# Kernel tuning notes

Measured on AMD Instinct MI355X. Metric: run time of the kernel, lower is better.

The kernel has to match this reference:

```python
import jax, jax.numpy as jnp
import numpy as np

HIDDEN = 20


def setup_inputs() -> dict:
    key = jax.random.key(0)
    ks = jax.random.split(key, 8)
    B, T = 8192, 2048
    x = jax.random.normal(ks[0], (B, T), dtype=jnp.float32)
    # linear1: 1 -> HIDDEN
    W1 = jax.random.normal(ks[1], (HIDDEN, 1), dtype=jnp.float32) * 0.5
    b1 = jax.random.normal(ks[2], (HIDDEN,), dtype=jnp.float32) * 0.1
    # LSTMCell(HIDDEN, HIDDEN): torch layout [4*H, H], gate order i,f,g,o
    W_ih = jax.random.normal(ks[3], (4 * HIDDEN, HIDDEN), dtype=jnp.float32) * 0.2
    W_hh = jax.random.normal(ks[4], (4 * HIDDEN, HIDDEN), dtype=jnp.float32) * 0.2
    b_ih = jax.random.normal(ks[5], (4 * HIDDEN,), dtype=jnp.float32) * 0.1
    b_hh = jax.random.normal(ks[6], (4 * HIDDEN,), dtype=jnp.float32) * 0.1
    # linear2: HIDDEN -> 1
    W2 = jax.random.normal(ks[7], (1, HIDDEN), dtype=jnp.float32) * 0.2
    b2 = jnp.zeros((1,), dtype=jnp.float32)
    return {"input": x, "W1": W1, "b1": b1, "W_ih": W_ih, "W_hh": W_hh,
            "b_ih": b_ih, "b_hh": b_hh, "W2": W2, "b2": b2}


def reference(input, W1, b1, W_ih, W_hh, b_ih, b_hh, W2, b2):
    B, T = input.shape
    h0 = jnp.zeros((B, HIDDEN), dtype=input.dtype)
    c0 = jnp.zeros((B, HIDDEN), dtype=input.dtype)

    def step(carry, x_t):
        h, c = carry
        # linear1 on scalar input: [B] -> [B, HIDDEN]
        hid = x_t[:, None] * W1[:, 0][None, :] + b1
        # LSTMCell gates, torch order: i, f, g, o
        gates = hid @ W_ih.T + b_ih + h @ W_hh.T + b_hh  # [B, 4H]
        i_g, f_g, g_g, o_g = jnp.split(gates, 4, axis=-1)
        c_new = jax.nn.sigmoid(f_g) * c + jax.nn.sigmoid(i_g) * jnp.tanh(g_g)
        h_new = jax.nn.sigmoid(o_g) * jnp.tanh(c_new)
        out = h_new @ W2.T + b2  # [B, 1]
        return (h_new, c_new), out[:, 0]

    xs = input.T  # [T, B]
    _, outs = jax.lax.scan(step, (h0, c0), xs)  # outs: [T, B]
    return outs.T  # [B, T]
```

## Files before the change

kernel.cpp:

```cpp
#include <hip/hip_runtime.h>


#define HID 20
#define ROWS_PER_WAVE 3
#define NTHREADS 64
#define L2E 1.4426950408889634f

typedef _Float16 v2h __attribute__((ext_vector_type(2)));

__device__ __forceinline__ float exp2_hw(float v) { return __builtin_amdgcn_exp2f(v); }
__device__ __forceinline__ float rcp_hw(float v)  { return __builtin_amdgcn_rcpf(v); }

__device__ __forceinline__ float sig_s(float gs) {
    return rcp_hw(1.0f + exp2_hw(-gs));
}

__device__ __forceinline__ float dot2(v2h w, v2h h, float acc) {
#if __has_builtin(__builtin_amdgcn_fdot2)
    return __builtin_amdgcn_fdot2(w, h, acc, false);
#else
    asm("v_dot2_f32_f16 %0, %1, %2, %0" : "+v"(acc) : "v"(w), "v"(h));
    return acc;
#endif
}

__device__ __forceinline__ v2h u2h(unsigned u) {
    v2h r; __builtin_memcpy(&r, &u, 4); return r;
}

__global__ __attribute__((amdgpu_flat_work_group_size(NTHREADS, NTHREADS),
                          amdgpu_waves_per_eu(3, 3)))
void lstm_wave(
        const float* __restrict__ x,
        const float* __restrict__ W1,
        const float* __restrict__ b1,
        const float* __restrict__ W_ih,
        const float* __restrict__ W_hh,
        const float* __restrict__ b_ih,
        const float* __restrict__ b_hh,
        const float* __restrict__ W2,
        const float* __restrict__ b2,
        float* __restrict__ out,
        const int B, const int T)
{
    const int lane = threadIdx.x;
    const int lrow = lane / HID;
    const int m    = lane % HID;
    const bool outlane = (lrow == 3) && (m < ROWS_PER_WAVE);
    const int rslot = (lrow == 3) ? m : lrow;
    const long rowbase = (long)blockIdx.x * ROWS_PER_WAVE;
    const long row = rowbase + ((lrow == 3) ? (long)((m < 3) ? m : 0) : (long)lrow);
    const long arow = (row < B) ? row : (B - 1);
    const bool ovalid = outlane && (row < B);

    __shared__ __align__(16) _Float16 hbuf[ROWS_PER_WAVE + 1][32];

    float u[4], v[4];
    if (lrow < 3) {
#pragma unroll
        for (int g = 0; g < 4; ++g) {
            const int j = g * HID + m;
            const float s = (g == 2) ? (2.0f * L2E) : L2E;
            float uu = 0.f, vv = 0.f;
#pragma unroll
            for (int k = 0; k < HID; ++k) {
                const float wi = W_ih[j * HID + k];
                uu += wi * W1[k];
                vv += wi * b1[k];
            }
            u[g] = s * uu;
            v[g] = s * (vv + b_ih[j] + b_hh[j]);
        }
    } else {
#pragma unroll
        for (int g = 0; g < 4; ++g) { u[g] = 0.f; v[g] = 0.f; }
        v[0] = b2[0];
    }

    v2h whh[4][HID / 2];
    if (lrow < 3) {
#pragma unroll
        for (int g = 0; g < 4; ++g) {
            const int j = g * HID + m;
            const float s = (g == 2) ? (2.0f * L2E) : L2E;
#pragma unroll
            for (int kk = 0; kk < HID / 2; ++kk) {
                v2h w;
                w.x = (_Float16)(s * W_hh[j * HID + 2 * kk]);
                w.y = (_Float16)(s * W_hh[j * HID + 2 * kk + 1]);
                whh[g][kk] = w;
            }
        }
    } else {
#pragma unroll
        for (int kk = 0; kk < HID / 2; ++kk) {
            v2h w;
            w.x = (_Float16)W2[2 * kk];
            w.y = (_Float16)W2[2 * kk + 1];
            whh[0][kk] = w;
            whh[1][kk] = (v2h)(_Float16)0;
            whh[2][kk] = (v2h)(_Float16)0;
            whh[3][kk] = (v2h)(_Float16)0;
        }
    }

#pragma unroll
    for (int g = 0; g < 4; ++g)
#pragma unroll
        for (int kk = 0; kk < HID / 2; ++kk)
            asm volatile("" : "+v"(whh[g][kk]));

    float cs = 0.f;

    ((_Float16*)hbuf)[lane]      = (_Float16)0;
    ((_Float16*)hbuf)[lane + 64] = (_Float16)0;

    const float* __restrict__ xrow = x   + arow * T;
    float* __restrict__       orow = out + arow * T;

    const uint4* __restrict__ rdp4 = (const uint4*)&hbuf[rslot][0];
    const uint2* __restrict__ rdp2 = (const uint2*)&hbuf[rslot][16];
    _Float16* __restrict__    wrp  = &hbuf[lrow][m];

    v2h hp[HID / 2];
#pragma unroll
    for (int q = 0; q < HID / 2; ++q) hp[q] = (v2h)(_Float16)0;

    float4 xq = *(const float4*)&xrow[0];
    float4 xq_next;
    float4 obuf = make_float4(0.f, 0.f, 0.f, 0.f);

#define BODY(XV, OSLOT)                                                         \
    {                                                                           \
        const float xv = (XV);                                                  \
        float a0 = fmaf(xv, u[0], v[0]);                                        \
        float a1 = fmaf(xv, u[1], v[1]);                                        \
        float a2 = fmaf(xv, u[2], v[2]);                                        \
        float a3 = fmaf(xv, u[3], v[3]);                                        \
        _Pragma("unroll")                                                       \
        for (int q = 0; q < HID / 2; ++q) {                                     \
            a0 = dot2(whh[0][q], hp[q], a0);                                    \
            a1 = dot2(whh[1][q], hp[q], a1);                                    \
            a2 = dot2(whh[2][q], hp[q], a2);                                    \
            a3 = dot2(whh[3][q], hp[q], a3);                                    \
        }                                                                       \
        __builtin_amdgcn_s_setprio(1);                                          \
        OSLOT = a0;                                                             \
        const float fg  = sig_s(a1);                                            \
        const float e0i = exp2_hw(-a0);                                         \
        const float e2  = exp2_hw(a2);                                          \
        const float P1  = (1.0f + e0i) * (1.0f + e2);                           \
        const float igg = (2.0f * L2E) * (e2 - 1.0f) * rcp_hw(P1);              \
        cs = fg * cs + igg;                                                     \
        const float e3i = exp2_hw(-a3);                                         \
        const float ec  = exp2_hw(cs);                                          \
        const float P2  = (1.0f + e3i) * (1.0f + ec);                           \
        *wrp = (_Float16)((ec - 1.0f) * rcp_hw(P2));                            \
        const uint4 Ra = rdp4[0];                                               \
        const uint4 Rb = rdp4[1];                                               \
        const uint2 Rc = *rdp2;                                                 \
        __builtin_amdgcn_s_setprio(0);                                          \
        hp[0] = u2h(Ra.x); hp[1] = u2h(Ra.y); hp[2] = u2h(Ra.z);                \
        hp[3] = u2h(Ra.w); hp[4] = u2h(Rb.x); hp[5] = u2h(Rb.y);                \
        hp[6] = u2h(Rb.z); hp[7] = u2h(Rb.w); hp[8] = u2h(Rc.x);                \
        hp[9] = u2h(Rc.y);                                                      \
    }

    for (int t = 0; t < T; t += 4) {
        const int tp = (t + 4 < T) ? (t + 4) : t;
        xq_next = *(const float4*)&xrow[tp];

        BODY(xq.x, obuf.w)
        if (t >= 4 && ovalid) *(float4*)&orow[t - 4] = obuf;
        BODY(xq.y, obuf.x)
        BODY(xq.z, obuf.y)
        BODY(xq.w, obuf.z)

        xq = xq_next;
    }

    {
        float o = v[0];
#pragma unroll
        for (int q = 0; q < HID / 2; ++q)
            o = dot2(whh[0][q], hp[q], o);
        obuf.w = o;
        if (ovalid) *(float4*)&orow[T - 4] = obuf;
    }
#undef BODY
}

extern "C" void kernel_launch(void* const* d_in, const int* in_sizes, int n_in,
                              void* d_out, int out_size, void* d_ws, size_t ws_size,
                              hipStream_t stream) {
    (void)n_in; (void)d_ws; (void)ws_size; (void)out_size;
    const float* x    = (const float*)d_in[0];
    const float* W1   = (const float*)d_in[1];
    const float* b1   = (const float*)d_in[2];
    const float* W_ih = (const float*)d_in[3];
    const float* W_hh = (const float*)d_in[4];
    const float* b_ih = (const float*)d_in[5];
    const float* b_hh = (const float*)d_in[6];
    const float* W2   = (const float*)d_in[7];
    const float* b2   = (const float*)d_in[8];
    float* out        = (float*)d_out;

    const int B = 8192;
    const int T = in_sizes[0] / B;
    const int grid = (B + ROWS_PER_WAVE - 1) / ROWS_PER_WAVE;

    lstm_wave<<<grid, NTHREADS, 0, stream>>>(x, W1, b1, W_ih, W_hh, b_ih, b_hh, W2, b2, out, B, T);
}
```

Measured before the change: 957.6 us.

## Pack six batch rows per wave with two hidden units per lane

Remaps lanes so each lane owns two hidden units (10 lanes per row), fitting six batch rows per 64-lane wave instead of three. The output projection is folded into every lane's dot loop, and hidden states are exchanged as packed half2 words in LDS. This halves the number of waves and the serial per-step overhead per row, but doubles per-lane register weights and dependent work. Occupancy is lowered to 2 waves per EU to make room for the larger register footprint.

Measured after the change: 1.251 ms. 30.6% more time.

```diff
diff --git a/kernel.cpp b/kernel.cpp
--- a/kernel.cpp
+++ b/kernel.cpp
@@ -2,7 +2,8 @@
 
 
 #define HID 20
-#define ROWS_PER_WAVE 3
+#define LPR 10
+#define RPW 6
 #define NTHREADS 64
 #define L2E 1.4426950408889634f
 
@@ -27,9 +28,12 @@
 __device__ __forceinline__ v2h u2h(unsigned u) {
     v2h r; __builtin_memcpy(&r, &u, 4); return r;
 }
+__device__ __forceinline__ unsigned h2u(v2h h) {
+    unsigned r; __builtin_memcpy(&r, &h, 4); return r;
+}
 
 __global__ __attribute__((amdgpu_flat_work_group_size(NTHREADS, NTHREADS),
-                          amdgpu_waves_per_eu(3, 3)))
+                          amdgpu_waves_per_eu(2, 2)))
 void lstm_wave(
         const float* __restrict__ x,
         const float* __restrict__ W1,
@@ -44,118 +48,156 @@
         const int B, const int T)
 {
     const int lane = threadIdx.x;
-    const int lrow = lane / HID;
-    const int m    = lane % HID;
-    const bool outlane = (lrow == 3) && (m < ROWS_PER_WAVE);
-    const int rslot = (lrow == 3) ? m : lrow;
-    const long rowbase = (long)blockIdx.x * ROWS_PER_WAVE;
-    const long row = rowbase + ((lrow == 3) ? (long)((m < 3) ? m : 0) : (long)lrow);
-    const long arow = (row < B) ? row : (B - 1);
-    const bool ovalid = outlane && (row < B);
-
-    __shared__ __align__(16) _Float16 hbuf[ROWS_PER_WAVE + 1][32];
-
-    float u[4], v[4];
-    if (lrow < 3) {
+    const int r    = lane / LPR;
+    const int mlo  = lane % LPR;
+    const bool gatelane = (r < RPW);
+    const int rslot = gatelane ? r : (lane - 60);
+
+    int outr = -1;
+    if (lane >= 60)      outr = lane - 60;
+    else if (lane == 40) outr = 4;
+    else if (lane == 50) outr = 5;
+    const bool has_out = (outr >= 0);
+
+    const long rowbase = (long)blockIdx.x * RPW;
+    const long xr   = rowbase + rslot;
+    const long arow = (xr < B) ? xr : (B - 1);
+    const long orw  = has_out ? (rowbase + outr) : 0;
+    const long oarw = (orw < B) ? orw : (B - 1);
+    const bool ovalid = has_out && (orw < B);
+
+    __shared__ __align__(16) unsigned hbuf[RPW + 1][12];
+
+    float u[4][2], v[4][2];
+    v2h   whh[4][2][LPR];
+    v2h   w2[LPR];
+    float ob = 0.f;
+
+    if (gatelane) {
 #pragma unroll
         for (int g = 0; g < 4; ++g) {
-            const int j = g * HID + m;
             const float s = (g == 2) ? (2.0f * L2E) : L2E;
-            float uu = 0.f, vv = 0.f;
-#pragma unroll
-            for (int k = 0; k < HID; ++k) {
-                const float wi = W_ih[j * HID + k];
-                uu += wi * W1[k];
-                vv += wi * b1[k];
-            }
-            u[g] = s * uu;
-            v[g] = s * (vv + b_ih[j] + b_hh[j]);
-        }
-    } else {
-#pragma unroll
-        for (int g = 0; g < 4; ++g) { u[g] = 0.f; v[g] = 0.f; }
-        v[0] = b2[0];
-    }
-
-    v2h whh[4][HID / 2];
-    if (lrow < 3) {
-#pragma unroll
-        for (int g = 0; g < 4; ++g) {
-            const int j = g * HID + m;
-            const float s = (g == 2) ? (2.0f * L2E) : L2E;
-#pragma unroll
-            for (int kk = 0; kk < HID / 2; ++kk) {
-                v2h w;
-                w.x = (_Float16)(s * W_hh[j * HID + 2 * kk]);
-                w.y = (_Float16)(s * W_hh[j * HID + 2 * kk + 1]);
-                whh[g][kk] = w;
+#pragma unroll
+            for (int un = 0; un < 2; ++un) {
+                const int j = g * HID + mlo + un * 10;
+                float uu = 0.f, vv = 0.f;
+#pragma unroll
+                for (int k = 0; k < HID; ++k) {
+                    const float wi = W_ih[j * HID + k];
+                    uu += wi * W1[k];
+                    vv += wi * b1[k];
+                }
+                u[g][un] = s * uu;
+                v[g][un] = s * (vv + b_ih[j] + b_hh[j]);
+#pragma unroll
+                for (int q = 0; q < LPR; ++q) {
+                    v2h w;
+                    w.x = (_Float16)(s * W_hh[j * HID + q]);
+                    w.y = (_Float16)(s * W_hh[j * HID + q + 10]);
+                    whh[g][un][q] = w;
+                }
             }
         }
     } else {
 #pragma unroll
-        for (int kk = 0; kk < HID / 2; ++kk) {
+        for (int g = 0; g < 4; ++g)
+#pragma unroll
+            for (int un = 0; un < 2; ++un) {
+                u[g][un] = 0.f; v[g][un] = 0.f;
+#pragma unroll
+                for (int q = 0; q < LPR; ++q) whh[g][un][q] = (v2h)(_Float16)0;
+            }
+    }
+    if (has_out) {
+#pragma unroll
+        for (int q = 0; q < LPR; ++q) {
             v2h w;
-            w.x = (_Float16)W2[2 * kk];
-            w.y = (_Float16)W2[2 * kk + 1];
-            whh[0][kk] = w;
-            whh[1][kk] = (v2h)(_Float16)0;
-            whh[2][kk] = (v2h)(_Float16)0;
-            whh[3][kk] = (v2h)(_Float16)0;
+            w.x = (_Float16)W2[q];
+            w.y = (_Float16)W2[q + 10];
+            w2[q] = w;
         }
+        ob = b2[0];
+    } else {
+#pragma unroll
+        for (int q = 0; q < LPR; ++q) w2[q] = (v2h)(_Float16)0;
     }
 
 #pragma unroll
     for (int g = 0; g < 4; ++g)
 #pragma unroll
-        for (int kk = 0; kk < HID / 2; ++kk)
-            asm volatile("" : "+v"(whh[g][kk]));
-
-    float cs = 0.f;
-
-    ((_Float16*)hbuf)[lane]      = (_Float16)0;
-    ((_Float16*)hbuf)[lane + 64] = (_Float16)0;
+        for (int un = 0; un < 2; ++un)
+#pragma unroll
+            for (int q = 0; q < LPR; ++q)
+                asm volatile("" : "+v"(whh[g][un][q]));
+#pragma unroll
+    for (int q = 0; q < LPR; ++q) asm volatile("" : "+v"(w2[q]));
+
+    float csL = 0.f, csH = 0.f;
+
+    ((unsigned*)hbuf)[lane] = 0u;
+    if (lane < 20) ((unsigned*)hbuf)[lane + 64] = 0u;
 
     const float* __restrict__ xrow = x   + arow * T;
-    float* __restrict__       orow = out + arow * T;
+    float* __restrict__       orow = out + oarw * T;
 
     const uint4* __restrict__ rdp4 = (const uint4*)&hbuf[rslot][0];
-    const uint2* __restrict__ rdp2 = (const uint2*)&hbuf[rslot][16];
-    _Float16* __restrict__    wrp  = &hbuf[lrow][m];
-
-    v2h hp[HID / 2];
-#pragma unroll
-    for (int q = 0; q < HID / 2; ++q) hp[q] = (v2h)(_Float16)0;
+    const uint2* __restrict__ rdp2 = (const uint2*)&hbuf[rslot][8];
+    unsigned* __restrict__    wrp  = &hbuf[r][mlo];
+
+    v2h hp[LPR];
+#pragma unroll
+    for (int q = 0; q < LPR; ++q) hp[q] = (v2h)(_Float16)0;
 
     float4 xq = *(const float4*)&xrow[0];
     float4 xq_next;
     float4 obuf = make_float4(0.f, 0.f, 0.f, 0.f);
 
+#define UNIT_ACT(AI, AF, AG, AO, CS, HOUT)                                      \
+    {                                                                           \
+        const float fg  = sig_s(AF);                                            \
+        const float e0i = exp2_hw(-(AI));                                       \
+        const float e2  = exp2_hw(AG);                                          \
+        const float P1  = (1.0f + e0i) * (1.0f + e2);                           \
+        const float igg = (2.0f * L2E) * (e2 - 1.0f) * rcp_hw(P1);              \
+        CS = fg * CS + igg;                                                     \
+        const float e3i = exp2_hw(-(AO));                                       \
+        const float ec  = exp2_hw(CS);                                          \
+        const float P2  = (1.0f + e3i) * (1.0f + ec);                           \
+        HOUT = (ec - 1.0f) * rcp_hw(P2);                                        \
+    }
+
 #define BODY(XV, OSLOT)                                                         \
     {                                                                           \
         const float xv = (XV);                                                  \
-        float a0 = fmaf(xv, u[0], v[0]);                                        \
-        float a1 = fmaf(xv, u[1], v[1]);                                        \
-        float a2 = fmaf(xv, u[2], v[2]);                                        \
-        float a3 = fmaf(xv, u[3], v[3]);                                        \
+        float a00 = fmaf(xv, u[0][0], v[0][0]);                                 \
+        float a01 = fmaf(xv, u[0][1], v[0][1]);                                 \
+        float a10 = fmaf(xv, u[1][0], v[1][0]);                                 \
+        float a11 = fmaf(xv, u[1][1], v[1][1]);                                 \
+        float a20 = fmaf(xv, u[2][0], v[2][0]);                                 \
+        float a21 = fmaf(xv, u[2][1], v[2][1]);                                 \
+        float a30 = fmaf(xv, u[3][0], v[3][0]);                                 \
+        float a31 = fmaf(xv, u[3][1], v[3][1]);                                 \
+        float o   = ob;                                                         \
         _Pragma("unroll")                                                       \
-        for (int q = 0; q < HID / 2; ++q) {                                     \
-            a0 = dot2(whh[0][q], hp[q], a0);                                    \
-            a1 = dot2(whh[1][q], hp[q], a1);                                    \
-            a2 = dot2(whh[2][q], hp[q], a2);                                    \
-            a3 = dot2(whh[3][q], hp[q], a3);                                    \
+        for (int q = 0; q < LPR; ++q) {                                         \
+            const v2h hq = hp[q];                                               \
+            a00 = dot2(whh[0][0][q], hq, a00);                                  \
+            a01 = dot2(whh[0][1][q], hq, a01);                                  \
+            a10 = dot2(whh[1][0][q], hq, a10);                                  \
+            a11 = dot2(whh[1][1][q], hq, a11);                                  \
+            a20 = dot2(whh[2][0][q], hq, a20);                                  \
+            a21 = dot2(whh[2][1][q], hq, a21);                                  \
+            a30 = dot2(whh[3][0][q], hq, a30);                                  \
+            a31 = dot2(whh[3][1][q], hq, a31);                                  \
+            o   = dot2(w2[q],        hq, o);                                    \
         }                                                                       \
+        OSLOT = o;                                                              \
         __builtin_amdgcn_s_setprio(1);                                          \
-        OSLOT = a0;                                                             \
-        const float fg  = sig_s(a1);                                            \
-        const float e0i = exp2_hw(-a0);                                         \
-        const float e2  = exp2_hw(a2);                                          \
-        const float P1  = (1.0f + e0i) * (1.0f + e2);                           \
-        const float igg = (2.0f * L2E) * (e2 - 1.0f) * rcp_hw(P1);              \
-        cs = fg * cs + igg;                                                     \
-        const float e3i = exp2_hw(-a3);                                         \
-        const float ec  = exp2_hw(cs);                                          \
-        const float P2  = (1.0f + e3i) * (1.0f + ec);                           \
-        *wrp = (_Float16)((ec - 1.0f) * rcp_hw(P2));                            \
+        float hL, hH;                                                           \
+        UNIT_ACT(a00, a10, a20, a30, csL, hL)                                   \
+        UNIT_ACT(a01, a11, a21, a31, csH, hH)                                   \
+        v2h hpk; hpk.x = (_Float16)hL; hpk.y = (_Float16)hH;                    \
+        *wrp = h2u(hpk);                                                        \
         const uint4 Ra = rdp4[0];                                               \
         const uint4 Rb = rdp4[1];                                               \
         const uint2 Rc = *rdp2;                                                 \
@@ -180,14 +222,15 @@
     }
 
     {
-        float o = v[0];
-#pragma unroll
-        for (int q = 0; q < HID / 2; ++q)
-            o = dot2(whh[0][q], hp[q], o);
+        float o = ob;
+#pragma unroll
+        for (int q = 0; q < LPR; ++q)
+            o = dot2(w2[q], hp[q], o);
         obuf.w = o;
         if (ovalid) *(float4*)&orow[T - 4] = obuf;
     }
 #undef BODY
+#undef UNIT_ACT
 }
 
 extern "C" void kernel_launch(void* const* d_in, const int* in_sizes, int n_in,
@@ -207,7 +250,7 @@
 
     const int B = 8192;
     const int T = in_sizes[0] / B;
-    const int grid = (B + ROWS_PER_WAVE - 1) / ROWS_PER_WAVE;
+    const int grid = (B + RPW - 1) / RPW;
 
     lstm_wave<<<grid, NTHREADS, 0, stream>>>(x, W1, b1, W_ih, W_hh, b_ih, b_hh, W2, b2, out, B, T);
 }
```
